# Optimization experiments

Hardware: AMD Instinct MI355X
Metric: run time of the kernel (lower is better)

Reference implementation:

```python
import jax, jax.numpy as jnp
from jax import lax
import numpy as np

ARG_NAMES = ('x w1 b1 bn1_g bn1_b bn1_m bn1_v w2 b2 bn2_g bn2_b bn2_m bn2_v w3 b3 w4 b4 '
             'attn_w attn_b attn_u g0_w1 g0_b1 g0_w2 g0_b2 g1_w1 g1_b1 g1_w2 g1_b2 '
             'g2_w1 g2_b1 g2_w2 g2_b2 c_w1 c_b1 c_w2 c_b2 c_w3 c_b3 c_w4 c_b4').split()


def _conv1d(x, w, b, stride, pad):
    # x: [N, C, L], w: [O, I, K]
    y = lax.conv_general_dilated(x, w, (stride,), [(pad, pad)],
                                 dimension_numbers=('NCH', 'OIH', 'NCH'))
    return y + b[None, :, None]


def _bn(x, g, b, m, v, eps=1e-5):
    # eval-mode BatchNorm1d over channel dim of [N, C, L]
    inv = g / jnp.sqrt(v + eps)
    return (x - m[None, :, None]) * inv[None, :, None] + b[None, :, None]


def _forward(x, w1, b1, bn1_g, bn1_b, bn1_m, bn1_v, w2, b2, bn2_g, bn2_b, bn2_m, bn2_v,
             w3, b3, w4, b4, attn_w, attn_b, attn_u,
             g0_w1, g0_b1, g0_w2, g0_b2, g1_w1, g1_b1, g1_w2, g1_b2,
             g2_w1, g2_b1, g2_w2, g2_b2,
             c_w1, c_b1, c_w2, c_b2, c_w3, c_b3, c_w4, c_b4):
    B, S, C, T = x.shape  # [batch, crops, channels=64, time=400]
    h = x.reshape(-1, C, T)
    # CNN stack (dropout = identity in eval)
    h = _bn(jax.nn.elu(_conv1d(h, w1, b1, 2, 1)), bn1_g, bn1_b, bn1_m, bn1_v)   # [N,64,192]
    h = _bn(jax.nn.elu(_conv1d(h, w2, b2, 2, 0)), bn2_g, bn2_b, bn2_m, bn2_v)   # [N,64,87]
    h = jax.nn.elu(_conv1d(h, w3, b3, 1, 0))                                    # [N,64,82]
    h = lax.reduce_window(h, 0.0, lax.add, (1, 1, 3), (1, 1, 2), 'VALID') / 3.0  # [N,64,40]
    h = jax.nn.elu(_conv1d(h, w4, b4, 1, 0))                                    # [N,64,35]
    h = h.reshape(B, S, C, -1)  # [B, S, 64, 35]
    # Attention pooling over the crop dim (dim=1), sum=True
    v = jnp.tanh(jnp.einsum('bsch,hd->bscd', h, attn_w) + attn_b)
    alphas = jax.nn.softmax(jnp.einsum('bscd,d->bsc', v, attn_u), axis=1)
    h = jax.nn.elu((h * alphas[..., None]).sum(axis=1))  # [B, 64, 35]
    # GIN over complete 64-node graph (self-loops included, eps=0):
    # aggregation per node == sum over all nodes of the graph
    def gin(h, W1, B1, W2, B2):
        agg = h + h.sum(axis=1, keepdims=True)
        return jax.nn.relu(agg @ W1 + B1) @ W2 + B2
    h = jax.nn.relu(gin(h, g0_w1, g0_b1, g0_w2, g0_b2))
    h = jax.nn.relu(gin(h, g1_w1, g1_b1, g1_w2, g1_b2))
    h = gin(h, g2_w1, g2_b1, g2_w2, g2_b2)  # no act after last layer
    # Classifier
    f = h.reshape(B, -1)  # [B, 2240]
    f = jax.nn.elu(f @ c_w1 + c_b1)
    f = jax.nn.elu(f @ c_w2 + c_b2)
    f = jax.nn.elu(f @ c_w3 + c_b3)
    return f @ c_w4 + c_b4  # [B, 2]


def setup_inputs() -> dict:
    key = jax.random.key(0)
    ks = iter(jax.random.split(key, 64))
    def rn(shape, s=0.05):
        return jax.random.normal(next(ks), shape, dtype=jnp.float32) * s
    d = {}
    d['x'] = jax.random.normal(next(ks), (32, 16, 64, 400), dtype=jnp.float32)
    d['w1'] = rn((64, 64, 20)); d['b1'] = rn((64,))
    d['bn1_g'] = jnp.ones((64,), jnp.float32); d['bn1_b'] = jnp.zeros((64,), jnp.float32)
    d['bn1_m'] = jnp.zeros((64,), jnp.float32); d['bn1_v'] = jnp.ones((64,), jnp.float32)
    d['w2'] = rn((64, 64, 20)); d['b2'] = rn((64,))
    d['bn2_g'] = jnp.ones((64,), jnp.float32); d['bn2_b'] = jnp.zeros((64,), jnp.float32)
    d['bn2_m'] = jnp.zeros((64,), jnp.float32); d['bn2_v'] = jnp.ones((64,), jnp.float32)
    d['w3'] = rn((64, 64, 6)); d['b3'] = rn((64,))
    d['w4'] = rn((64, 64, 6)); d['b4'] = rn((64,))
    d['attn_w'] = rn((35, 256), 0.1); d['attn_b'] = rn((256,), 0.1); d['attn_u'] = rn((256,), 0.1)
    d['g0_w1'] = rn((35, 256)); d['g0_b1'] = rn((256,))
    d['g0_w2'] = rn((256, 256)); d['g0_b2'] = rn((256,))
    d['g1_w1'] = rn((256, 256)); d['g1_b1'] = rn((256,))
    d['g1_w2'] = rn((256, 256)); d['g1_b2'] = rn((256,))
    d['g2_w1'] = rn((256, 35)); d['g2_b1'] = rn((35,))
    d['g2_w2'] = rn((35, 35)); d['g2_b2'] = rn((35,))
    d['c_w1'] = rn((2240, 256)); d['c_b1'] = rn((256,))
    d['c_w2'] = rn((256, 64)); d['c_b2'] = rn((64,))
    d['c_w3'] = rn((64, 16)); d['c_b3'] = rn((16,))
    d['c_w4'] = rn((16, 2)); d['c_b4'] = rn((2,))
    return d


def reference(x, w1, b1, bn1_g, bn1_b, bn1_m, bn1_v, w2, b2, bn2_g, bn2_b, bn2_m, bn2_v,
              w3, b3, w4, b4, attn_w, attn_b, attn_u,
              g0_w1, g0_b1, g0_w2, g0_b2, g1_w1, g1_b1, g1_w2, g1_b2,
              g2_w1, g2_b1, g2_w2, g2_b2,
              c_w1, c_b1, c_w2, c_b2, c_w3, c_b3, c_w4, c_b4):
    return _forward(x, w1, b1, bn1_g, bn1_b, bn1_m, bn1_v, w2, b2, bn2_g, bn2_b, bn2_m, bn2_v,
                    w3, b3, w4, b4, attn_w, attn_b, attn_u,
                    g0_w1, g0_b1, g0_w2, g0_b2, g1_w1, g1_b1, g1_w2, g1_b2,
                    g2_w1, g2_b1, g2_w2, g2_b2,
                    c_w1, c_b1, c_w2, c_b2, c_w3, c_b3, c_w4, c_b4)
```

## Files before the change

kernel.cpp:

```cpp
#include <hip/hip_runtime.h>
#include <math.h>

typedef __attribute__((ext_vector_type(8))) __bf16 bf16x8;
typedef __attribute__((ext_vector_type(4))) __bf16 bf16x4;
typedef __attribute__((ext_vector_type(4))) float f32x4;

__device__ __forceinline__ float elu_f(float v) {
    return v > 0.f ? v : (expf(v) - 1.f);
}

__global__ __launch_bounds__(256) void prep_weights(
    const float* __restrict__ w1, const float* __restrict__ w2,
    const float* __restrict__ w3, const float* __restrict__ w4,
    __bf16* __restrict__ t1, __bf16* __restrict__ t2,
    __bf16* __restrict__ t3, __bf16* __restrict__ t4)
{
    int idx = blockIdx.x * 256 + threadIdx.x;
    if (idx < 81920) {
        int k = idx / 4096, r = idx - k * 4096, co = r >> 6, ci = r & 63;
        t1[idx] = (__bf16)w1[(co * 64 + ci) * 20 + k];
    } else if (idx < 163840) {
        int j = idx - 81920;
        int k = j / 4096, r = j - k * 4096, co = r >> 6, ci = r & 63;
        t2[j] = (__bf16)w2[(co * 64 + ci) * 20 + k];
    } else if (idx < 188416) {
        int j = idx - 163840;
        int k = j / 4096, r = j - k * 4096, co = r >> 6, ci = r & 63;
        t3[j] = (__bf16)w3[(co * 64 + ci) * 6 + k];
    } else if (idx < 212992) {
        int j = idx - 188416;
        int k = j / 4096, r = j - k * 4096, co = r >> 6, ci = r & 63;
        t4[j] = (__bf16)w4[(co * 64 + ci) * 6 + k];
    }
}

__global__ __launch_bounds__(256) void prep_tr(
    const float* __restrict__ g0w1, const float* __restrict__ g0w2,
    const float* __restrict__ g1w1, const float* __restrict__ g1w2,
    const float* __restrict__ g2w1, const float* __restrict__ g2w2,
    __bf16* __restrict__ d0, __bf16* __restrict__ d1, __bf16* __restrict__ d2,
    __bf16* __restrict__ d3, __bf16* __restrict__ d4, __bf16* __restrict__ d5)
{
    int bid = blockIdx.x;
    const float* src; __bf16* dst; int K, O, Kpad, Opad, tile;
    if (bid < 4)       { src = g0w1; dst = d0; K = 35;   O = 256; Kpad = 64;   Opad = 256; tile = bid; }
    else if (bid < 20) { src = g0w2; dst = d1; K = 256;  O = 256; Kpad = 256;  Opad = 256; tile = bid - 4; }
    else if (bid < 36) { src = g1w1; dst = d2; K = 256;  O = 256; Kpad = 256;  Opad = 256; tile = bid - 20; }
    else if (bid < 52) { src = g1w2; dst = d3; K = 256;  O = 256; Kpad = 256;  Opad = 256; tile = bid - 36; }
    else if (bid < 56) { src = g2w1; dst = d4; K = 256;  O = 35;  Kpad = 256;  Opad = 64;  tile = bid - 52; }
    else               { src = g2w2; dst = d5; K = 35;   O = 35;  Kpad = 64;   Opad = 64;  tile = 0; }
    int ktiles = Kpad >> 6;
    int ot = tile / ktiles, kt = tile - ot * ktiles;
    int k0 = kt * 64, o0 = ot * 64;
    size_t LOFF = (size_t)Opad * Kpad;
    __shared__ float tl[64][68];
    int c = threadIdx.x & 63, rr = threadIdx.x >> 6;
    #pragma unroll
    for (int it = 0; it < 16; ++it) {
        int r = rr + it * 4;
        int kk = k0 + r, oo = o0 + c;
        tl[r][c] = (kk < K && oo < O) ? src[(size_t)kk * O + oo] : 0.f;
    }
    __syncthreads();
    #pragma unroll
    for (int it = 0; it < 16; ++it) {
        int r = rr + it * 4;
        float v = tl[c][r];
        __bf16 hi = (__bf16)v;
        float lo = v - (float)hi;
        size_t pos = (size_t)(o0 + r) * Kpad + k0 + c;
        dst[pos] = hi;
        dst[LOFF + pos] = (__bf16)lo;
    }
}

template<int K, int STRIDE, int PAD, bool DO_BN, int IMODE,
         int NPB, int TPN, int LIN, int LOUT, int KCHUNK >
__global__ __launch_bounds__(NPB * TPN * 64, 2) void conv_mfma(
    const void* __restrict__ xin, const __bf16* __restrict__ wT,
    const float* __restrict__ bias,
    const float* __restrict__ bn_g, const float* __restrict__ bn_b,
    const float* __restrict__ bn_m, const float* __restrict__ bn_v,
    __bf16* __restrict__ y)
{
    constexpr int THREADS = NPB * TPN * 64;
    constexpr int TBLK  = TPN * 48;
    constexpr int VSPAN = STRIDE * (TBLK - 1) + K;
    constexpr int NBUF  = (STRIDE == 2) ? 2 : 1;
    constexpr int ROWS  = (VSPAN + NBUF - 1) / NBUF;
    __shared__ __align__(16) __bf16 sx[NPB * NBUF * ROWS * 72];

    const int tid = threadIdx.x;
    const int nb  = blockIdx.x * NPB;

    if constexpr (IMODE == 0) {
        const float* xg = (const float*)xin + (size_t)nb * 64 * LIN;
        constexpr int NZROWS = PAD + (VSPAN - LIN - PAD);
        if (tid < NZROWS * 64) {
            int zr = tid >> 6;
            int v = (zr < PAD) ? zr : (LIN + PAD + zr - PAD);
            sx[((v & (NBUF - 1)) * ROWS + (v >> (NBUF - 1))) * 72 + (tid & 63)] = (__bf16)0.f;
        }
        constexpr int J4 = LIN / 4;
        constexpr int ITEMS = 16 * J4;
        constexpr int ITER = (ITEMS + THREADS - 1) / THREADS;
        #pragma unroll
        for (int it = 0; it < ITER; ++it) {
            int idx = it * THREADS + tid;
            if (ITEMS % THREADS == 0 || idx < ITEMS) {
                int jj = idx & 3;
                int g  = (idx >> 2) & 15;
                int q  = (idx >> 6) * 4 + jj;
                const float* xp = xg + (size_t)(4 * g) * LIN + 4 * q;
                float fa[4][4];
                #pragma unroll
                for (int u = 0; u < 4; ++u)
                    *(float4*)&fa[u][0] = *(const float4*)(xp + (size_t)u * LIN);
                #pragma unroll
                for (int e = 0; e < 4; ++e) {
                    int v = 4 * q + e + PAD;
                    bf16x4 wv = { (__bf16)fa[0][e], (__bf16)fa[1][e],
                                  (__bf16)fa[2][e], (__bf16)fa[3][e] };
                    *(bf16x4*)&sx[((v & (NBUF - 1)) * ROWS + (v >> (NBUF - 1))) * 72 + 4 * g] = wv;
                }
            }
        }
    }
    __syncthreads();

    const int wave = tid >> 6, lane = tid & 63;
    const int n_l  = wave / TPN, tile = wave - n_l * TPN;
    const int m    = lane & 15, quad = lane >> 4;
    const __bf16* sxn = sx + (size_t)n_l * NBUF * ROWS * 72;

    f32x4 acc[3][4];
    #pragma unroll
    for (int mi = 0; mi < 3; ++mi)
        #pragma unroll
        for (int nj = 0; nj < 4; ++nj)
            acc[mi][nj] = (f32x4){0.f, 0.f, 0.f, 0.f};

    const __bf16* wbase = wT + (size_t)m * 64 + quad * 8;
    bf16x8 bcur[2][4];
    #pragma unroll
    for (int s = 0; s < 2; ++s)
        #pragma unroll
        for (int nj = 0; nj < 4; ++nj)
            bcur[s][nj] = *(const bf16x8*)(wbase + nj * (16 * 64) + s * 32);

    for (int kp = 0; kp < K; ++kp) {
        const int kn = (kp + 1 < K) ? kp + 1 : kp;
        bf16x8 bnxt[2][4];
        #pragma unroll
        for (int s = 0; s < 2; ++s)
            #pragma unroll
            for (int nj = 0; nj < 4; ++nj)
                bnxt[s][nj] = *(const bf16x8*)(wbase + (size_t)kn * 4096 + nj * (16 * 64) + s * 32);

        const int xbuf   = (STRIDE == 2) ? (kp & 1) : 0;
        const int rowoff = (STRIDE == 2) ? (kp >> 1) : kp;
        const __bf16* abase = sxn + ((size_t)xbuf * ROWS + tile * 48 + m + rowoff) * 72;
        #pragma unroll
        for (int s = 0; s < 2; ++s) {
            bf16x8 af[3];
            #pragma unroll
            for (int mi = 0; mi < 3; ++mi)
                af[mi] = *(const bf16x8*)(abase + mi * (16 * 72) + s * 32 + quad * 8);
            #pragma unroll
            for (int mi = 0; mi < 3; ++mi)
                #pragma unroll
                for (int nj = 0; nj < 4; ++nj)
                    acc[mi][nj] = __builtin_amdgcn_mfma_f32_16x16x32_bf16(
                        af[mi], bcur[s][nj], acc[mi][nj], 0, 0, 0);
        }
        #pragma unroll
        for (int s = 0; s < 2; ++s)
            #pragma unroll
            for (int nj = 0; nj < 4; ++nj)
                bcur[s][nj] = bnxt[s][nj];
    }

    #pragma unroll
    for (int nj = 0; nj < 4; ++nj) {
        const int co = nj * 16 + m;
        const float bi = bias[co];
        float scale = 1.f, shift = 0.f;
        if constexpr (DO_BN) {
            float inv = bn_g[co] / sqrtf(bn_v[co] + 1e-5f);
            scale = inv; shift = bn_b[co] - bn_m[co] * inv;
        }
        #pragma unroll
        for (int mi = 0; mi < 3; ++mi) {
            #pragma unroll
            for (int r = 0; r < 4; ++r) {
                int t = tile * 48 + mi * 16 + quad * 4 + r;
                if (t < LOUT) {
                    float v = acc[mi][nj][r] + bi;
                    v = elu_f(v);
                    if constexpr (DO_BN) v = v * scale + shift;
                    y[((size_t)(nb + n_l) * LOUT + t) * 64 + co] = (__bf16)v;
                }
            }
        }
    }
}

__global__ __launch_bounds__(256, 2) void conv234_fused(
    const __bf16* __restrict__ h1,
    const __bf16* __restrict__ wT2, const float* __restrict__ b2,
    const float* __restrict__ bn2g, const float* __restrict__ bn2b,
    const float* __restrict__ bn2m, const float* __restrict__ bn2v,
    const __bf16* __restrict__ wT3, const float* __restrict__ b3,
    const __bf16* __restrict__ wT4, const float* __restrict__ b4,
    __bf16* __restrict__ h4)
{
    __shared__ __align__(16) __bf16 bufA[2 * 96 * 72];
    __shared__ __align__(16) __bf16 bufB[87 * 72];

    const int tid = threadIdx.x;
    const int n = blockIdx.x;
    const int wave = tid >> 6, lane = tid & 63;
    const int m = lane & 15, quad = lane >> 4;
    const int th = wave >> 1;
    const int coh = (wave & 1) * 32;

    {
        const __bf16* src = h1 + (size_t)n * 192 * 64;
        #pragma unroll
        for (int it = 0; it < 6; ++it) {
            int idx = it * 256 + tid;
            int v = idx >> 3, c8 = (idx & 7) * 8;
            *(uint4*)(bufA + ((size_t)(v & 1) * 96 + (v >> 1)) * 72 + c8) =
                *(const uint4*)(src + (size_t)v * 64 + c8);
        }
    }
    __syncthreads();

    {
        f32x4 acc[3][2];
        #pragma unroll
        for (int mi = 0; mi < 3; ++mi)
            #pragma unroll
            for (int nj = 0; nj < 2; ++nj)
                acc[mi][nj] = (f32x4){0.f, 0.f, 0.f, 0.f};

        const __bf16* wb = wT2 + (size_t)(coh + m) * 64 + quad * 8;
        bf16x8 bcur[2][2];
        #pragma unroll
        for (int s = 0; s < 2; ++s)
            #pragma unroll
            for (int nj = 0; nj < 2; ++nj)
                bcur[s][nj] = *(const bf16x8*)(wb + nj * (16 * 64) + s * 32);

        for (int kp = 0; kp < 20; ++kp) {
            const int kn = (kp + 1 < 20) ? kp + 1 : kp;
            bf16x8 bnxt[2][2];
            #pragma unroll
            for (int s = 0; s < 2; ++s)
                #pragma unroll
                for (int nj = 0; nj < 2; ++nj)
                    bnxt[s][nj] = *(const bf16x8*)(wb + (size_t)kn * 4096 + nj * (16 * 64) + s * 32);

            const int buf = kp & 1, rowoff = kp >> 1;
            const int r0 = th * 48 + m + rowoff;
            #pragma unroll
            for (int s = 0; s < 2; ++s) {
                bf16x8 af[3];
                #pragma unroll
                for (int mi = 0; mi < 3; ++mi) {
                    int rr = r0 + mi * 16; if (rr > 95) rr = 95;
                    af[mi] = *(const bf16x8*)(bufA + ((size_t)buf * 96 + rr) * 72 + s * 32 + quad * 8);
                }
                #pragma unroll
                for (int mi = 0; mi < 3; ++mi)
                    #pragma unroll
                    for (int nj = 0; nj < 2; ++nj)
                        acc[mi][nj] = __builtin_amdgcn_mfma_f32_16x16x32_bf16(
                            af[mi], bcur[s][nj], acc[mi][nj], 0, 0, 0);
            }
            #pragma unroll
            for (int s = 0; s < 2; ++s)
                #pragma unroll
                for (int nj = 0; nj < 2; ++nj)
                    bcur[s][nj] = bnxt[s][nj];
        }

        #pragma unroll
        for (int nj = 0; nj < 2; ++nj) {
            const int co = coh + nj * 16 + m;
            const float bi = b2[co];
            float inv = bn2g[co] / sqrtf(bn2v[co] + 1e-5f);
            float shift = bn2b[co] - bn2m[co] * inv;
            #pragma unroll
            for (int mi = 0; mi < 3; ++mi)
                #pragma unroll
                for (int r = 0; r < 4; ++r) {
                    int t = th * 48 + mi * 16 + quad * 4 + r;
                    if (t < 87) {
                        float v = elu_f(acc[mi][nj][r] + bi) * inv + shift;
                        bufB[t * 72 + co] = (__bf16)v;
                    }
                }
        }
    }
    __syncthreads();

    {
        f32x4 acc[3][2];
        #pragma unroll
        for (int mi = 0; mi < 3; ++mi)
            #pragma unroll
            for (int nj = 0; nj < 2; ++nj)
                acc[mi][nj] = (f32x4){0.f, 0.f, 0.f, 0.f};

        const __bf16* wb = wT3 + (size_t)(coh + m) * 64 + quad * 8;
        bf16x8 bcur[2][2];
        #pragma unroll
        for (int s = 0; s < 2; ++s)
            #pragma unroll
            for (int nj = 0; nj < 2; ++nj)
                bcur[s][nj] = *(const bf16x8*)(wb + nj * (16 * 64) + s * 32);

        #pragma unroll
        for (int kp = 0; kp < 6; ++kp) {
            const int kn = (kp + 1 < 6) ? kp + 1 : kp;
            bf16x8 bnxt[2][2];
            #pragma unroll
            for (int s = 0; s < 2; ++s)
                #pragma unroll
                for (int nj = 0; nj < 2; ++nj)
                    bnxt[s][nj] = *(const bf16x8*)(wb + (size_t)kn * 4096 + nj * (16 * 64) + s * 32);

            const int r0 = th * 48 + m + kp;
            #pragma unroll
            for (int s = 0; s < 2; ++s) {
                bf16x8 af[3];
                #pragma unroll
                for (int mi = 0; mi < 3; ++mi) {
                    int rr = r0 + mi * 16; if (rr > 86) rr = 86;
                    af[mi] = *(const bf16x8*)(bufB + (size_t)rr * 72 + s * 32 + quad * 8);
                }
                #pragma unroll
                for (int mi = 0; mi < 3; ++mi)
                    #pragma unroll
                    for (int nj = 0; nj < 2; ++nj)
                        acc[mi][nj] = __builtin_amdgcn_mfma_f32_16x16x32_bf16(
                            af[mi], bcur[s][nj], acc[mi][nj], 0, 0, 0);
            }
            #pragma unroll
            for (int s = 0; s < 2; ++s)
                #pragma unroll
                for (int nj = 0; nj < 2; ++nj)
                    bcur[s][nj] = bnxt[s][nj];
        }

        #pragma unroll
        for (int nj = 0; nj < 2; ++nj) {
            const int co = coh + nj * 16 + m;
            const float bi = b3[co];
            #pragma unroll
            for (int mi = 0; mi < 3; ++mi)
                #pragma unroll
                for (int r = 0; r < 4; ++r) {
                    int t = th * 48 + mi * 16 + quad * 4 + r;
                    if (t < 82)
                        bufA[t * 72 + co] = (__bf16)elu_f(acc[mi][nj][r] + bi);
                }
        }
    }
    __syncthreads();

    #pragma unroll
    for (int it = 0; it < 10; ++it) {
        int idx = it * 256 + tid;
        int t = idx >> 6, co = idx & 63;
        float v = ((float)bufA[(2 * t) * 72 + co] + (float)bufA[(2 * t + 1) * 72 + co] +
                   (float)bufA[(2 * t + 2) * 72 + co]) * (1.f / 3.f);
        bufB[t * 72 + co] = (__bf16)v;
    }
    __syncthreads();

    {
        const int co0 = wave * 16;
        f32x4 acc4[3];
        #pragma unroll
        for (int mi = 0; mi < 3; ++mi)
            acc4[mi] = (f32x4){0.f, 0.f, 0.f, 0.f};

        const __bf16* wb = wT4 + (size_t)(co0 + m) * 64 + quad * 8;
        bf16x8 bcur[2];
        #pragma unroll
        for (int s = 0; s < 2; ++s)
            bcur[s] = *(const bf16x8*)(wb + s * 32);

        #pragma unroll
        for (int kp = 0; kp < 6; ++kp) {
            const int kn = (kp + 1 < 6) ? kp + 1 : kp;
            bf16x8 bnxt[2];
            #pragma unroll
            for (int s = 0; s < 2; ++s)
                bnxt[s] = *(const bf16x8*)(wb + (size_t)kn * 4096 + s * 32);

            const int r0 = m + kp;
            #pragma unroll
            for (int s = 0; s < 2; ++s) {
                bf16x8 af[3];
                #pragma unroll
                for (int mi = 0; mi < 3; ++mi) {
                    int rr = r0 + mi * 16; if (rr > 39) rr = 39;
                    af[mi] = *(const bf16x8*)(bufB + (size_t)rr * 72 + s * 32 + quad * 8);
                }
                #pragma unroll
                for (int mi = 0; mi < 3; ++mi)
                    acc4[mi] = __builtin_amdgcn_mfma_f32_16x16x32_bf16(
                        af[mi], bcur[s], acc4[mi], 0, 0, 0);
            }
            #pragma unroll
            for (int s = 0; s < 2; ++s)
                bcur[s] = bnxt[s];
        }

        const int co = co0 + m;
        const float bi = b4[co];
        #pragma unroll
        for (int mi = 0; mi < 3; ++mi)
            #pragma unroll
            for (int r = 0; r < 4; ++r) {
                int t = mi * 16 + quad * 4 + r;
                if (t < 35)
                    h4[((size_t)n * 35 + t) * 64 + co] = (__bf16)elu_f(acc4[mi][r] + bi);
            }
    }
}

__global__ __launch_bounds__(256) void attn_pool_k(
    const __bf16* __restrict__ h, const float* __restrict__ W,
    const float* __restrict__ ab, const float* __restrict__ u,
    float* __restrict__ out)
{
    __shared__ float sW[35 * 256];
    __shared__ float sh[4][16 * 35 + 5];
    const int tid = threadIdx.x;
    const int pair0 = blockIdx.x * 4;
    for (int i = tid; i < 35 * 256; i += 256) sW[i] = W[i];
    for (int i = tid; i < 4 * 560; i += 256) {
        int q = i / 560, r = i - q * 560;
        int s = r / 35, t = r - s * 35;
        int bc = pair0 + q, b = bc >> 6, c = bc & 63;
        sh[q][s * 35 + t] = (float)h[(((size_t)b * 16 + s) * 35 + t) * 64 + c];
    }
    __syncthreads();

    const int wave = tid >> 6, lane = tid & 63;
    const int bc = pair0 + wave;
    const float* shw = sh[wave];

    float myu[4], myb[4];
    #pragma unroll
    for (int p = 0; p < 4; ++p) { myu[p] = u[lane + 64 * p]; myb[p] = ab[lane + 64 * p]; }

    float dot[16][4];
    #pragma unroll
    for (int s = 0; s < 16; ++s)
        #pragma unroll
        for (int p = 0; p < 4; ++p) dot[s][p] = myb[p];

    for (int t = 0; t < 35; ++t) {
        float w0 = sW[t * 256 + lane];
        float w1 = sW[t * 256 + lane + 64];
        float w2 = sW[t * 256 + lane + 128];
        float w3 = sW[t * 256 + lane + 192];
        #pragma unroll
        for (int s = 0; s < 16; ++s) {
            float hv = shw[s * 35 + t];
            dot[s][0] = fmaf(hv, w0, dot[s][0]);
            dot[s][1] = fmaf(hv, w1, dot[s][1]);
            dot[s][2] = fmaf(hv, w2, dot[s][2]);
            dot[s][3] = fmaf(hv, w3, dot[s][3]);
        }
    }

    float sc[16];
    #pragma unroll
    for (int s = 0; s < 16; ++s) {
        float v = tanhf(dot[s][0]) * myu[0] + tanhf(dot[s][1]) * myu[1]
                + tanhf(dot[s][2]) * myu[2] + tanhf(dot[s][3]) * myu[3];
        #pragma unroll
        for (int off = 1; off < 64; off <<= 1) v += __shfl_xor(v, off, 64);
        sc[s] = v;
    }

    float mx = sc[0];
    #pragma unroll
    for (int s = 1; s < 16; ++s) mx = fmaxf(mx, sc[s]);
    float e[16], sum = 0.f;
    #pragma unroll
    for (int s = 0; s < 16; ++s) { e[s] = expf(sc[s] - mx); sum += e[s]; }
    float inv = 1.f / sum;

    if (lane < 35) {
        float acc = 0.f;
        #pragma unroll
        for (int s = 0; s < 16; ++s) acc = fmaf(shw[s * 35 + lane], e[s] * inv, acc);
        out[(size_t)bc * 35 + lane] = elu_f(acc);
    }
}

#define APLANE (64 * 264)

__device__ __forceinline__ void gin_gemm_dev(
    const __bf16* As,
    const __bf16* __restrict__ Wg, int Kpad, int wlo, int Kout,
    const float* __restrict__ bias,
    int mode, __bf16* Ad, float* __restrict__ outg)
{
    const int lane = threadIdx.x & 63;
    const int wave = threadIdx.x >> 6;
    const int o0 = wave * 32;
    if (o0 >= ((Kout + 63) & ~63)) return;
    const int m = lane & 15, quad = lane >> 4;

    f32x4 acc[4][2];
    #pragma unroll
    for (int mi = 0; mi < 4; ++mi)
        #pragma unroll
        for (int nj = 0; nj < 2; ++nj)
            acc[mi][nj] = (f32x4){0.f, 0.f, 0.f, 0.f};

    for (int k0 = 0; k0 < Kpad; k0 += 32) {
        bf16x8 ah[4], al[4], bh[2], bl[2];
        #pragma unroll
        for (int mi = 0; mi < 4; ++mi) {
            const __bf16* ap = As + (size_t)(mi * 16 + m) * 264 + k0 + quad * 8;
            ah[mi] = *(const bf16x8*)ap;
            al[mi] = *(const bf16x8*)(ap + APLANE);
        }
        #pragma unroll
        for (int nj = 0; nj < 2; ++nj) {
            const __bf16* wp = Wg + (size_t)(o0 + nj * 16 + m) * Kpad + k0 + quad * 8;
            bh[nj] = *(const bf16x8*)wp;
            bl[nj] = *(const bf16x8*)(wp + wlo);
        }
        #pragma unroll
        for (int mi = 0; mi < 4; ++mi)
            #pragma unroll
            for (int nj = 0; nj < 2; ++nj) {
                acc[mi][nj] = __builtin_amdgcn_mfma_f32_16x16x32_bf16(
                    al[mi], bh[nj], acc[mi][nj], 0, 0, 0);
                acc[mi][nj] = __builtin_amdgcn_mfma_f32_16x16x32_bf16(
                    ah[mi], bl[nj], acc[mi][nj], 0, 0, 0);
                acc[mi][nj] = __builtin_amdgcn_mfma_f32_16x16x32_bf16(
                    ah[mi], bh[nj], acc[mi][nj], 0, 0, 0);
            }
    }

    #pragma unroll
    for (int nj = 0; nj < 2; ++nj) {
        const int o = o0 + nj * 16 + m;
        const bool ovalid = (o < Kout);
        const float bi = ovalid ? bias[o] : 0.f;
        float v[4][4];
        #pragma unroll
        for (int mi = 0; mi < 4; ++mi)
            #pragma unroll
            for (int r = 0; r < 4; ++r)
                v[mi][r] = acc[mi][nj][r] + bi;
        if (mode == 2) {
            if (ovalid) {
                #pragma unroll
                for (int mi = 0; mi < 4; ++mi)
                    #pragma unroll
                    for (int r = 0; r < 4; ++r)
                        outg[(size_t)(mi * 16 + quad * 4 + r) * Kout + o] = v[mi][r];
            }
        } else {
            float s = 0.f;
            #pragma unroll
            for (int mi = 0; mi < 4; ++mi)
                #pragma unroll
                for (int r = 0; r < 4; ++r) {
                    float rv = ovalid ? fmaxf(v[mi][r], 0.f) : 0.f;
                    v[mi][r] = rv;
                    s += rv;
                }
            if (mode == 1) {
                s += __shfl_xor(s, 16, 64);
                s += __shfl_xor(s, 32, 64);
            } else {
                s = 0.f;
            }
            #pragma unroll
            for (int mi = 0; mi < 4; ++mi)
                #pragma unroll
                for (int r = 0; r < 4; ++r) {
                    float a = v[mi][r] + s;
                    __bf16 hi = (__bf16)a;
                    size_t pos = (size_t)(mi * 16 + quad * 4 + r) * 264 + o;
                    Ad[pos] = hi;
                    Ad[APLANE + pos] = (__bf16)(a - (float)hi);
                }
        }
    }
}

__global__ __launch_bounds__(512) void gin_fused(
    const float* __restrict__ ha,
    const __bf16* __restrict__ gW0a, const __bf16* __restrict__ gW0b,
    const __bf16* __restrict__ gW1a, const __bf16* __restrict__ gW1b,
    const __bf16* __restrict__ gW2a, const __bf16* __restrict__ gW2b,
    const float* __restrict__ b0a, const float* __restrict__ b0b,
    const float* __restrict__ b1a, const float* __restrict__ b1b,
    const float* __restrict__ b2a, const float* __restrict__ b2b,
    float* __restrict__ H3)
{
    const int b = blockIdx.x, tid = threadIdx.x;
    __shared__ __align__(16) __bf16 sA[2][2 * APLANE];
    __shared__ float sS[64];
    const float* hab = ha + (size_t)b * 2240;

    if (tid < 64) {
        float s = 0.f;
        if (tid < 35)
            for (int n = 0; n < 64; ++n) s += hab[n * 35 + tid];
        sS[tid] = s;
    }
    __syncthreads();
    for (int idx = tid; idx < 64 * 64; idx += 512) {
        int n = idx >> 6, k = idx & 63;
        float a = (k < 35) ? hab[n * 35 + k] + sS[k] : 0.f;
        __bf16 hi = (__bf16)a;
        sA[0][n * 264 + k] = hi;
        sA[0][APLANE + n * 264 + k] = (__bf16)(a - (float)hi);
    }
    __syncthreads();

    gin_gemm_dev(sA[0], gW0a, 64,  16384, 256, b0a, 0, sA[1], nullptr); __syncthreads();
    gin_gemm_dev(sA[1], gW0b, 256, 65536, 256, b0b, 1, sA[0], nullptr); __syncthreads();
    gin_gemm_dev(sA[0], gW1a, 256, 65536, 256, b1a, 0, sA[1], nullptr); __syncthreads();
    gin_gemm_dev(sA[1], gW1b, 256, 65536, 256, b1b, 1, sA[0], nullptr); __syncthreads();
    gin_gemm_dev(sA[0], gW2a, 256, 16384, 35,  b2a, 0, sA[1], nullptr); __syncthreads();
    gin_gemm_dev(sA[1], gW2b, 64,  4096,  35,  b2b, 2, nullptr, H3 + (size_t)b * 2240);
}

__global__ __launch_bounds__(256) void cls1_part_k(
    const float* __restrict__ H3, const float* __restrict__ w1,
    float* __restrict__ s1p)
{
    const int b  = blockIdx.x;
    const int kc = blockIdx.y;
    const int k0 = kc * 140;
    __shared__ float sH[140];
    const int tid = threadIdx.x;
    if (tid < 140) sH[tid] = H3[(size_t)b * 2240 + k0 + tid];
    __syncthreads();
    const int o = (tid >> 6) * 64 + (tid & 63);
    float a0 = 0.f, a1 = 0.f, a2 = 0.f, a3 = 0.f;
    const float* wr = w1 + (size_t)k0 * 256 + o;
    #pragma unroll
    for (int k = 0; k < 140; k += 4) {
        a0 = fmaf(sH[k],     wr[(size_t)k * 256],       a0);
        a1 = fmaf(sH[k + 1], wr[(size_t)(k + 1) * 256], a1);
        a2 = fmaf(sH[k + 2], wr[(size_t)(k + 2) * 256], a2);
        a3 = fmaf(sH[k + 3], wr[(size_t)(k + 3) * 256], a3);
    }
    s1p[((size_t)kc * 32 + b) * 256 + o] = a0 + a1 + a2 + a3;
}

__global__ __launch_bounds__(256) void cls234_k(
    const float* __restrict__ s1p, const float* __restrict__ b1,
    const float* __restrict__ w2, const float* __restrict__ b2,
    const float* __restrict__ w3, const float* __restrict__ b3,
    const float* __restrict__ w4, const float* __restrict__ b4,
    float* __restrict__ out)
{
    const int b = blockIdx.x, tid = threadIdx.x;
    __shared__ float s1[256];
    __shared__ float part[4][64];
    __shared__ float s2[64];
    __shared__ float s3[16];
    {
        float acc = b1[tid];
        #pragma unroll
        for (int kc = 0; kc < 16; ++kc)
            acc += s1p[((size_t)kc * 32 + b) * 256 + tid];
        s1[tid] = elu_f(acc);
    }
    __syncthreads();
    {
        int kg = tid >> 6, o = tid & 63;
        float acc = 0.f;
        for (int k = kg * 64; k < kg * 64 + 64; ++k)
            acc = fmaf(s1[k], w2[k * 64 + o], acc);
        part[kg][o] = acc;
    }
    __syncthreads();
    if (tid < 64) {
        float acc = part[0][tid] + part[1][tid] + part[2][tid] + part[3][tid] + b2[tid];
        s2[tid] = elu_f(acc);
    }
    __syncthreads();
    if (tid < 16) {
        float acc = b3[tid];
        for (int k = 0; k < 64; ++k) acc = fmaf(s2[k], w3[k * 16 + tid], acc);
        s3[tid] = elu_f(acc);
    }
    __syncthreads();
    if (tid < 2) {
        float acc = b4[tid];
        for (int k = 0; k < 16; ++k) acc = fmaf(s3[k], w4[k * 2 + tid], acc);
        out[b * 2 + tid] = acc;
    }
}

extern "C" void kernel_launch(void* const* d_in, const int* in_sizes, int n_in,
                              void* d_out, int out_size, void* d_ws, size_t ws_size,
                              hipStream_t stream)
{
    const float* x     = (const float*)d_in[0];
    const float* w1    = (const float*)d_in[1];
    const float* b1    = (const float*)d_in[2];
    const float* bn1_g = (const float*)d_in[3];
    const float* bn1_b = (const float*)d_in[4];
    const float* bn1_m = (const float*)d_in[5];
    const float* bn1_v = (const float*)d_in[6];
    const float* w2    = (const float*)d_in[7];
    const float* b2    = (const float*)d_in[8];
    const float* bn2_g = (const float*)d_in[9];
    const float* bn2_b = (const float*)d_in[10];
    const float* bn2_m = (const float*)d_in[11];
    const float* bn2_v = (const float*)d_in[12];
    const float* w3    = (const float*)d_in[13];
    const float* b3    = (const float*)d_in[14];
    const float* w4    = (const float*)d_in[15];
    const float* b4    = (const float*)d_in[16];
    const float* attn_w = (const float*)d_in[17];
    const float* attn_b = (const float*)d_in[18];
    const float* attn_u = (const float*)d_in[19];
    const float* g0_w1 = (const float*)d_in[20];
    const float* g0_b1 = (const float*)d_in[21];
    const float* g0_w2 = (const float*)d_in[22];
    const float* g0_b2 = (const float*)d_in[23];
    const float* g1_w1 = (const float*)d_in[24];
    const float* g1_b1 = (const float*)d_in[25];
    const float* g1_w2 = (const float*)d_in[26];
    const float* g1_b2 = (const float*)d_in[27];
    const float* g2_w1 = (const float*)d_in[28];
    const float* g2_b1 = (const float*)d_in[29];
    const float* g2_w2 = (const float*)d_in[30];
    const float* g2_b2 = (const float*)d_in[31];
    const float* c_w1  = (const float*)d_in[32];
    const float* c_b1  = (const float*)d_in[33];
    const float* c_w2  = (const float*)d_in[34];
    const float* c_b2  = (const float*)d_in[35];
    const float* c_w3  = (const float*)d_in[36];
    const float* c_b3  = (const float*)d_in[37];
    const float* c_w4  = (const float*)d_in[38];
    const float* c_b4  = (const float*)d_in[39];
    float* out = (float*)d_out;

    char* ws = (char*)d_ws;
    __bf16* wT1  = (__bf16*)(ws + 0);
    __bf16* wT2  = (__bf16*)(ws + 163840);
    __bf16* wT3  = (__bf16*)(ws + 327680);
    __bf16* wT4  = (__bf16*)(ws + 376832);
    __bf16* h1   = (__bf16*)(ws + 425984);
    __bf16* h4   = (__bf16*)(ws + 13008896);
    float*  ha   = (float*)(ws + 15302656);
    __bf16* gW0a = (__bf16*)(ws + 15589376);
    __bf16* gW0b = (__bf16*)(ws + 15654912);
    __bf16* gW1a = (__bf16*)(ws + 15917056);
    __bf16* gW1b = (__bf16*)(ws + 16179200);
    __bf16* gW2a = (__bf16*)(ws + 16441344);
    __bf16* gW2b = (__bf16*)(ws + 16506880);
    float*  H3   = (float*)(ws + 16523264);
    float*  s1p  = (float*)(ws + 16809984);

    prep_weights<<<dim3(832), dim3(256), 0, stream>>>(w1, w2, w3, w4, wT1, wT2, wT3, wT4);
    prep_tr<<<dim3(57), dim3(256), 0, stream>>>(g0_w1, g0_w2, g1_w1, g1_w2, g2_w1, g2_w2,
                                                gW0a, gW0b, gW1a, gW1b, gW2a, gW2b);

    conv_mfma<20, 2, 1, true, 0, 1, 4, 400, 192, 2><<<dim3(512), dim3(256), 0, stream>>>(
        x, wT1, b1, bn1_g, bn1_b, bn1_m, bn1_v, h1);

    conv234_fused<<<dim3(512), dim3(256), 0, stream>>>(
        h1, wT2, b2, bn2_g, bn2_b, bn2_m, bn2_v, wT3, b3, wT4, b4, h4);

    attn_pool_k<<<dim3(512), dim3(256), 0, stream>>>(h4, attn_w, attn_b, attn_u, ha);

    gin_fused<<<dim3(32), dim3(512), 0, stream>>>(
        ha, gW0a, gW0b, gW1a, gW1b, gW2a, gW2b,
        g0_b1, g0_b2, g1_b1, g1_b2, g2_b1, g2_b2, H3);

    cls1_part_k<<<dim3(32, 16), dim3(256), 0, stream>>>(H3, c_w1, s1p);
    cls234_k<<<dim3(32), dim3(256), 0, stream>>>(s1p, c_b1, c_w2, c_b2, c_w3, c_b3,
                                                 c_w4, c_b4, out);
}
```

Before: 326.7 us.

## Split conv work across waves by output channel with register-resident weights

Conv1 is rewritten so each wave owns 16 output channels and loops over four time tiles, holding all 20 taps of its weight slice in registers instead of streaming weights per tap. conv234_fused moves to 512 threads, with each wave owning one 16-channel slice per time half, and likewise preloads whole weight slices into registers. The goal is to cut repeated global weight loads and shrink per-wave accumulator state so more waves can hide latency. In exchange, the bw[20][2] arrays raise register pressure, which could lower occupancy or cause spills.

```diff
diff --git a/kernel.cpp b/kernel.cpp
--- a/kernel.cpp
+++ b/kernel.cpp
@@ -74,40 +74,33 @@
     }
 }
 
-template<int K, int STRIDE, int PAD, bool DO_BN, int IMODE,
-         int NPB, int TPN, int LIN, int LOUT, int KCHUNK >
-__global__ __launch_bounds__(NPB * TPN * 64, 2) void conv_mfma(
-    const void* __restrict__ xin, const __bf16* __restrict__ wT,
+__global__ __launch_bounds__(256, 2) void conv1_mfma(
+    const float* __restrict__ x, const __bf16* __restrict__ wT,
     const float* __restrict__ bias,
     const float* __restrict__ bn_g, const float* __restrict__ bn_b,
     const float* __restrict__ bn_m, const float* __restrict__ bn_v,
     __bf16* __restrict__ y)
 {
-    constexpr int THREADS = NPB * TPN * 64;
-    constexpr int TBLK  = TPN * 48;
-    constexpr int VSPAN = STRIDE * (TBLK - 1) + K;
-    constexpr int NBUF  = (STRIDE == 2) ? 2 : 1;
-    constexpr int ROWS  = (VSPAN + NBUF - 1) / NBUF;
-    __shared__ __align__(16) __bf16 sx[NPB * NBUF * ROWS * 72];
+    constexpr int LIN = 400, LOUT = 192, PAD = 1;
+    constexpr int ROWS = 201;
+    __shared__ __align__(16) __bf16 sx[2 * ROWS * 72];
 
     const int tid = threadIdx.x;
-    const int nb  = blockIdx.x * NPB;
-
-    if constexpr (IMODE == 0) {
-        const float* xg = (const float*)xin + (size_t)nb * 64 * LIN;
-        constexpr int NZROWS = PAD + (VSPAN - LIN - PAD);
-        if (tid < NZROWS * 64) {
-            int zr = tid >> 6;
-            int v = (zr < PAD) ? zr : (LIN + PAD + zr - PAD);
-            sx[((v & (NBUF - 1)) * ROWS + (v >> (NBUF - 1))) * 72 + (tid & 63)] = (__bf16)0.f;
-        }
-        constexpr int J4 = LIN / 4;
-        constexpr int ITEMS = 16 * J4;
-        constexpr int ITER = (ITEMS + THREADS - 1) / THREADS;
-        #pragma unroll
-        for (int it = 0; it < ITER; ++it) {
-            int idx = it * THREADS + tid;
-            if (ITEMS % THREADS == 0 || idx < ITEMS) {
+    const int n = blockIdx.x;
+    const int wave = tid >> 6, lane = tid & 63;
+    const int m = lane & 15, quad = lane >> 4;
+
+    {
+        const float* xg = x + (size_t)n * 64 * LIN;
+        if (tid < 128) {
+            int v = (tid >> 6) ? 401 : 0;
+            sx[((v & 1) * ROWS + (v >> 1)) * 72 + (tid & 63)] = (__bf16)0.f;
+        }
+        constexpr int ITEMS = 16 * (LIN / 4);
+        #pragma unroll
+        for (int it = 0; it < 7; ++it) {
+            int idx = it * 256 + tid;
+            if (idx < ITEMS) {
                 int jj = idx & 3;
                 int g  = (idx >> 2) & 15;
                 int q  = (idx >> 6) * 4 + jj;
@@ -121,91 +114,61 @@
                     int v = 4 * q + e + PAD;
                     bf16x4 wv = { (__bf16)fa[0][e], (__bf16)fa[1][e],
                                   (__bf16)fa[2][e], (__bf16)fa[3][e] };
-                    *(bf16x4*)&sx[((v & (NBUF - 1)) * ROWS + (v >> (NBUF - 1))) * 72 + 4 * g] = wv;
+                    *(bf16x4*)&sx[((v & 1) * ROWS + (v >> 1)) * 72 + 4 * g] = wv;
                 }
             }
         }
     }
-    __syncthreads();
-
-    const int wave = tid >> 6, lane = tid & 63;
-    const int n_l  = wave / TPN, tile = wave - n_l * TPN;
-    const int m    = lane & 15, quad = lane >> 4;
-    const __bf16* sxn = sx + (size_t)n_l * NBUF * ROWS * 72;
-
-    f32x4 acc[3][4];
-    #pragma unroll
-    for (int mi = 0; mi < 3; ++mi)
-        #pragma unroll
-        for (int nj = 0; nj < 4; ++nj)
-            acc[mi][nj] = (f32x4){0.f, 0.f, 0.f, 0.f};
-
-    const __bf16* wbase = wT + (size_t)m * 64 + quad * 8;
-    bf16x8 bcur[2][4];
-    #pragma unroll
-    for (int s = 0; s < 2; ++s)
-        #pragma unroll
-        for (int nj = 0; nj < 4; ++nj)
-            bcur[s][nj] = *(const bf16x8*)(wbase + nj * (16 * 64) + s * 32);
-
-    for (int kp = 0; kp < K; ++kp) {
-        const int kn = (kp + 1 < K) ? kp + 1 : kp;
-        bf16x8 bnxt[2][4];
+
+    const __bf16* wb = wT + (size_t)(wave * 16 + m) * 64 + quad * 8;
+    bf16x8 bw[20][2];
+    #pragma unroll
+    for (int kp = 0; kp < 20; ++kp)
         #pragma unroll
         for (int s = 0; s < 2; ++s)
-            #pragma unroll
-            for (int nj = 0; nj < 4; ++nj)
-                bnxt[s][nj] = *(const bf16x8*)(wbase + (size_t)kn * 4096 + nj * (16 * 64) + s * 32);
-
-        const int xbuf   = (STRIDE == 2) ? (kp & 1) : 0;
-        const int rowoff = (STRIDE == 2) ? (kp >> 1) : kp;
-        const __bf16* abase = sxn + ((size_t)xbuf * ROWS + tile * 48 + m + rowoff) * 72;
-        #pragma unroll
-        for (int s = 0; s < 2; ++s) {
-            bf16x8 af[3];
-            #pragma unroll
-            for (int mi = 0; mi < 3; ++mi)
-                af[mi] = *(const bf16x8*)(abase + mi * (16 * 72) + s * 32 + quad * 8);
-            #pragma unroll
-            for (int mi = 0; mi < 3; ++mi)
-                #pragma unroll
-                for (int nj = 0; nj < 4; ++nj)
-                    acc[mi][nj] = __builtin_amdgcn_mfma_f32_16x16x32_bf16(
-                        af[mi], bcur[s][nj], acc[mi][nj], 0, 0, 0);
-        }
-        #pragma unroll
-        for (int s = 0; s < 2; ++s)
-            #pragma unroll
-            for (int nj = 0; nj < 4; ++nj)
-                bcur[s][nj] = bnxt[s][nj];
-    }
-
-    #pragma unroll
-    for (int nj = 0; nj < 4; ++nj) {
-        const int co = nj * 16 + m;
-        const float bi = bias[co];
-        float scale = 1.f, shift = 0.f;
-        if constexpr (DO_BN) {
-            float inv = bn_g[co] / sqrtf(bn_v[co] + 1e-5f);
-            scale = inv; shift = bn_b[co] - bn_m[co] * inv;
-        }
-        #pragma unroll
-        for (int mi = 0; mi < 3; ++mi) {
+            bw[kp][s] = *(const bf16x8*)(wb + (size_t)kp * 4096 + s * 32);
+
+    __syncthreads();
+
+    const int co = wave * 16 + m;
+    const float bi = bias[co];
+    const float inv   = bn_g[co] / sqrtf(bn_v[co] + 1e-5f);
+    const float shift = bn_b[co] - bn_m[co] * inv;
+
+    for (int mo = 0; mo < 4; ++mo) {
+        f32x4 acc[3];
+        #pragma unroll
+        for (int mi = 0; mi < 3; ++mi) acc[mi] = (f32x4){0.f, 0.f, 0.f, 0.f};
+
+        #pragma unroll
+        for (int kp = 0; kp < 20; ++kp) {
+            const int buf = kp & 1, rowoff = kp >> 1;
+            const __bf16* abase = sx + ((size_t)buf * ROWS + mo * 48 + m + rowoff) * 72;
+            #pragma unroll
+            for (int s = 0; s < 2; ++s) {
+                bf16x8 af[3];
+                #pragma unroll
+                for (int mi = 0; mi < 3; ++mi)
+                    af[mi] = *(const bf16x8*)(abase + mi * (16 * 72) + s * 32 + quad * 8);
+                #pragma unroll
+                for (int mi = 0; mi < 3; ++mi)
+                    acc[mi] = __builtin_amdgcn_mfma_f32_16x16x32_bf16(
+                        af[mi], bw[kp][s], acc[mi], 0, 0, 0);
+            }
+        }
+
+        #pragma unroll
+        for (int mi = 0; mi < 3; ++mi)
             #pragma unroll
             for (int r = 0; r < 4; ++r) {
-                int t = tile * 48 + mi * 16 + quad * 4 + r;
-                if (t < LOUT) {
-                    float v = acc[mi][nj][r] + bi;
-                    v = elu_f(v);
-                    if constexpr (DO_BN) v = v * scale + shift;
-                    y[((size_t)(nb + n_l) * LOUT + t) * 64 + co] = (__bf16)v;
-                }
-            }
-        }
-    }
-}
-
-__global__ __launch_bounds__(256, 2) void conv234_fused(
+                int t = mo * 48 + mi * 16 + quad * 4 + r;
+                float v = elu_f(acc[mi][r] + bi) * inv + shift;
+                y[((size_t)n * LOUT + t) * 64 + co] = (__bf16)v;
+            }
+    }
+}
+
+__global__ __launch_bounds__(512, 2) void conv234_fused(
     const __bf16* __restrict__ h1,
     const __bf16* __restrict__ wT2, const float* __restrict__ b2,
     const float* __restrict__ bn2g, const float* __restrict__ bn2b,
@@ -221,14 +184,14 @@
     const int n = blockIdx.x;
     const int wave = tid >> 6, lane = tid & 63;
     const int m = lane & 15, quad = lane >> 4;
-    const int th = wave >> 1;
-    const int coh = (wave & 1) * 32;
+    const int th  = wave >> 2;
+    const int coq = wave & 3;
 
     {
         const __bf16* src = h1 + (size_t)n * 192 * 64;
         #pragma unroll
-        for (int it = 0; it < 6; ++it) {
-            int idx = it * 256 + tid;
+        for (int it = 0; it < 3; ++it) {
+            int idx = it * 512 + tid;
             int v = idx >> 3, c8 = (idx & 7) * 8;
             *(uint4*)(bufA + ((size_t)(v & 1) * 96 + (v >> 1)) * 72 + c8) =
                 *(const uint4*)(src + (size_t)v * 64 + c8);
@@ -237,30 +200,20 @@
     __syncthreads();
 
     {
-        f32x4 acc[3][2];
-        #pragma unroll
-        for (int mi = 0; mi < 3; ++mi)
-            #pragma unroll
-            for (int nj = 0; nj < 2; ++nj)
-                acc[mi][nj] = (f32x4){0.f, 0.f, 0.f, 0.f};
-
-        const __bf16* wb = wT2 + (size_t)(coh + m) * 64 + quad * 8;
-        bf16x8 bcur[2][2];
-        #pragma unroll
-        for (int s = 0; s < 2; ++s)
-            #pragma unroll
-            for (int nj = 0; nj < 2; ++nj)
-                bcur[s][nj] = *(const bf16x8*)(wb + nj * (16 * 64) + s * 32);
-
+        const __bf16* wb = wT2 + (size_t)(coq * 16 + m) * 64 + quad * 8;
+        bf16x8 bw[20][2];
+        #pragma unroll
+        for (int kp = 0; kp < 20; ++kp)
+            #pragma unroll
+            for (int s = 0; s < 2; ++s)
+                bw[kp][s] = *(const bf16x8*)(wb + (size_t)kp * 4096 + s * 32);
+
+        f32x4 acc[3];
+        #pragma unroll
+        for (int mi = 0; mi < 3; ++mi) acc[mi] = (f32x4){0.f, 0.f, 0.f, 0.f};
+
+        #pragma unroll
         for (int kp = 0; kp < 20; ++kp) {
-            const int kn = (kp + 1 < 20) ? kp + 1 : kp;
-            bf16x8 bnxt[2][2];
-            #pragma unroll
-            for (int s = 0; s < 2; ++s)
-                #pragma unroll
-                for (int nj = 0; nj < 2; ++nj)
-                    bnxt[s][nj] = *(const bf16x8*)(wb + (size_t)kn * 4096 + nj * (16 * 64) + s * 32);
-
             const int buf = kp & 1, rowoff = kp >> 1;
             const int r0 = th * 48 + m + rowoff;
             #pragma unroll
@@ -273,64 +226,43 @@
                 }
                 #pragma unroll
                 for (int mi = 0; mi < 3; ++mi)
-                    #pragma unroll
-                    for (int nj = 0; nj < 2; ++nj)
-                        acc[mi][nj] = __builtin_amdgcn_mfma_f32_16x16x32_bf16(
-                            af[mi], bcur[s][nj], acc[mi][nj], 0, 0, 0);
-            }
+                    acc[mi] = __builtin_amdgcn_mfma_f32_16x16x32_bf16(
+                        af[mi], bw[kp][s], acc[mi], 0, 0, 0);
+            }
+        }
+
+        const int co = coq * 16 + m;
+        const float bi = b2[co];
+        float inv = bn2g[co] / sqrtf(bn2v[co] + 1e-5f);
+        float shift = bn2b[co] - bn2m[co] * inv;
+        #pragma unroll
+        for (int mi = 0; mi < 3; ++mi)
+            #pragma unroll
+            for (int r = 0; r < 4; ++r) {
+                int t = th * 48 + mi * 16 + quad * 4 + r;
+                if (t < 87) {
+                    float v = elu_f(acc[mi][r] + bi) * inv + shift;
+                    bufB[t * 72 + co] = (__bf16)v;
+                }
+            }
+    }
+    __syncthreads();
+
+    {
+        const __bf16* wb = wT3 + (size_t)(coq * 16 + m) * 64 + quad * 8;
+        bf16x8 bw[6][2];
+        #pragma unroll
+        for (int kp = 0; kp < 6; ++kp)
             #pragma unroll
             for (int s = 0; s < 2; ++s)
-                #pragma unroll
-                for (int nj = 0; nj < 2; ++nj)
-                    bcur[s][nj] = bnxt[s][nj];
-        }
-
-        #pragma unroll
-        for (int nj = 0; nj < 2; ++nj) {
-            const int co = coh + nj * 16 + m;
-            const float bi = b2[co];
-            float inv = bn2g[co] / sqrtf(bn2v[co] + 1e-5f);
-            float shift = bn2b[co] - bn2m[co] * inv;
-            #pragma unroll
-            for (int mi = 0; mi < 3; ++mi)
-                #pragma unroll
-                for (int r = 0; r < 4; ++r) {
-                    int t = th * 48 + mi * 16 + quad * 4 + r;
-                    if (t < 87) {
-                        float v = elu_f(acc[mi][nj][r] + bi) * inv + shift;
-                        bufB[t * 72 + co] = (__bf16)v;
-                    }
-                }
-        }
-    }
-    __syncthreads();
-
-    {
-        f32x4 acc[3][2];
-        #pragma unroll
-        for (int mi = 0; mi < 3; ++mi)
-            #pragma unroll
-            for (int nj = 0; nj < 2; ++nj)
-                acc[mi][nj] = (f32x4){0.f, 0.f, 0.f, 0.f};
-
-        const __bf16* wb = wT3 + (size_t)(coh + m) * 64 + quad * 8;
-        bf16x8 bcur[2][2];
-        #pragma unroll
-        for (int s = 0; s < 2; ++s)
-            #pragma unroll
-            for (int nj = 0; nj < 2; ++nj)
-                bcur[s][nj] = *(const bf16x8*)(wb + nj * (16 * 64) + s * 32);
+                bw[kp][s] = *(const bf16x8*)(wb + (size_t)kp * 4096 + s * 32);
+
+        f32x4 acc[3];
+        #pragma unroll
+        for (int mi = 0; mi < 3; ++mi) acc[mi] = (f32x4){0.f, 0.f, 0.f, 0.f};
 
         #pragma unroll
         for (int kp = 0; kp < 6; ++kp) {
-            const int kn = (kp + 1 < 6) ? kp + 1 : kp;
-            bf16x8 bnxt[2][2];
-            #pragma unroll
-            for (int s = 0; s < 2; ++s)
-                #pragma unroll
-                for (int nj = 0; nj < 2; ++nj)
-                    bnxt[s][nj] = *(const bf16x8*)(wb + (size_t)kn * 4096 + nj * (16 * 64) + s * 32);
-
             const int r0 = th * 48 + m + kp;
             #pragma unroll
             for (int s = 0; s < 2; ++s) {
@@ -342,37 +274,27 @@
                 }
                 #pragma unroll
                 for (int mi = 0; mi < 3; ++mi)
-                    #pragma unroll
-                    for (int nj = 0; nj < 2; ++nj)
-                        acc[mi][nj] = __builtin_amdgcn_mfma_f32_16x16x32_bf16(
-                            af[mi], bcur[s][nj], acc[mi][nj], 0, 0, 0);
-            }
-            #pragma unroll
-            for (int s = 0; s < 2; ++s)
-                #pragma unroll
-                for (int nj = 0; nj < 2; ++nj)
-                    bcur[s][nj] = bnxt[s][nj];
-        }
-
-        #pragma unroll
-        for (int nj = 0; nj < 2; ++nj) {
-            const int co = coh + nj * 16 + m;
-            const float bi = b3[co];
-            #pragma unroll
-            for (int mi = 0; mi < 3; ++mi)
-                #pragma unroll
-                for (int r = 0; r < 4; ++r) {
-                    int t = th * 48 + mi * 16 + quad * 4 + r;
-                    if (t < 82)
-                        bufA[t * 72 + co] = (__bf16)elu_f(acc[mi][nj][r] + bi);
-                }
-        }
-    }
-    __syncthreads();
-
-    #pragma unroll
-    for (int it = 0; it < 10; ++it) {
-        int idx = it * 256 + tid;
+                    acc[mi] = __builtin_amdgcn_mfma_f32_16x16x32_bf16(
+                        af[mi], bw[kp][s], acc[mi], 0, 0, 0);
+            }
+        }
+
+        const int co = coq * 16 + m;
+        const float bi = b3[co];
+        #pragma unroll
+        for (int mi = 0; mi < 3; ++mi)
+            #pragma unroll
+            for (int r = 0; r < 4; ++r) {
+                int t = th * 48 + mi * 16 + quad * 4 + r;
+                if (t < 82)
+                    bufA[t * 72 + co] = (__bf16)elu_f(acc[mi][r] + bi);
+            }
+    }
+    __syncthreads();
+
+    #pragma unroll
+    for (int it = 0; it < 5; ++it) {
+        int idx = it * 512 + tid;
         int t = idx >> 6, co = idx & 63;
         float v = ((float)bufA[(2 * t) * 72 + co] + (float)bufA[(2 * t + 1) * 72 + co] +
                    (float)bufA[(2 * t + 2) * 72 + co]) * (1.f / 3.f);
@@ -380,27 +302,22 @@
     }
     __syncthreads();
 
-    {
+    if (wave < 4) {
         const int co0 = wave * 16;
+        const __bf16* wb = wT4 + (size_t)(co0 + m) * 64 + quad * 8;
+        bf16x8 bw[6][2];
+        #pragma unroll
+        for (int kp = 0; kp < 6; ++kp)
+            #pragma unroll
+            for (int s = 0; s < 2; ++s)
+                bw[kp][s] = *(const bf16x8*)(wb + (size_t)kp * 4096 + s * 32);
+
         f32x4 acc4[3];
         #pragma unroll
-        for (int mi = 0; mi < 3; ++mi)
-            acc4[mi] = (f32x4){0.f, 0.f, 0.f, 0.f};
-
-        const __bf16* wb = wT4 + (size_t)(co0 + m) * 64 + quad * 8;
-        bf16x8 bcur[2];
-        #pragma unroll
-        for (int s = 0; s < 2; ++s)
-            bcur[s] = *(const bf16x8*)(wb + s * 32);
+        for (int mi = 0; mi < 3; ++mi) acc4[mi] = (f32x4){0.f, 0.f, 0.f, 0.f};
 
         #pragma unroll
         for (int kp = 0; kp < 6; ++kp) {
-            const int kn = (kp + 1 < 6) ? kp + 1 : kp;
-            bf16x8 bnxt[2];
-            #pragma unroll
-            for (int s = 0; s < 2; ++s)
-                bnxt[s] = *(const bf16x8*)(wb + (size_t)kn * 4096 + s * 32);
-
             const int r0 = m + kp;
             #pragma unroll
             for (int s = 0; s < 2; ++s) {
@@ -413,11 +330,8 @@
                 #pragma unroll
                 for (int mi = 0; mi < 3; ++mi)
                     acc4[mi] = __builtin_amdgcn_mfma_f32_16x16x32_bf16(
-                        af[mi], bcur[s], acc4[mi], 0, 0, 0);
-            }
-            #pragma unroll
-            for (int s = 0; s < 2; ++s)
-                bcur[s] = bnxt[s];
+                        af[mi], bw[kp][s], acc4[mi], 0, 0, 0);
+            }
         }
 
         const int co = co0 + m;
@@ -779,10 +693,10 @@
     prep_tr<<<dim3(57), dim3(256), 0, stream>>>(g0_w1, g0_w2, g1_w1, g1_w2, g2_w1, g2_w2,
                                                 gW0a, gW0b, gW1a, gW1b, gW2a, gW2b);
 
-    conv_mfma<20, 2, 1, true, 0, 1, 4, 400, 192, 2><<<dim3(512), dim3(256), 0, stream>>>(
+    conv1_mfma<<<dim3(512), dim3(256), 0, stream>>>(
         x, wT1, b1, bn1_g, bn1_b, bn1_m, bn1_v, h1);
 
-    conv234_fused<<<dim3(512), dim3(256), 0, stream>>>(
+    conv234_fused<<<dim3(512), dim3(512), 0, stream>>>(
         h1, wT2, b2, bn2_g, bn2_b, bn2_m, bn2_v, wT3, b3, wT4, b4, h4);
 
     attn_pool_k<<<dim3(512), dim3(256), 0, stream>>>(h4, attn_w, attn_b, attn_u, ha);
```

Measured after the change: 300.8 us. -7.9%, faster.
